# Kernel tuning notes

Measured on AMD Instinct MI355X. Metric: run time of the kernel, lower is better.

Reference implementation:

```python
import jax, jax.numpy as jnp
import numpy as np

B, S, D = 2, 2048, 1024
H = 16
HD = D // H  # 64


def setup_inputs() -> dict:
    key = jax.random.key(0)
    k = jax.random.split(key, 6)
    s = 0.02
    return {
        "x": jax.random.normal(k[0], (B, S, D), dtype=jnp.float32),
        "wq": jax.random.normal(k[1], (D, D), dtype=jnp.float32) * s,
        "wk": jax.random.normal(k[2], (D, D), dtype=jnp.float32) * s,
        "wv": jax.random.normal(k[3], (D, D), dtype=jnp.float32) * s,
        "wo": jax.random.normal(k[4], (D, D), dtype=jnp.float32) * s,
        "bo": jnp.zeros((D,), dtype=jnp.float32),
    }


def reference(x, wq, wk, wv, wo, bo):
    b, n, d = x.shape
    # nn.Linear: y = x @ W.T (qkv_bias=False)
    def proj(w):
        y = jnp.einsum('bnd,od->bno', x, w)
        return y.reshape(b, n, H, HD).transpose(0, 2, 1, 3)  # (b, H, n, hd)
    q, k, v = proj(wq), proj(wk), proj(wv)
    scores = jnp.einsum('bhqd,bhkd->bhqk', q, k) / jnp.sqrt(jnp.float32(HD))
    # NOTE: source code slices the causal mask but never applies it; softmax is unmasked.
    attn = jax.nn.softmax(scores, axis=-1)
    # dropout p=0.0 -> identity
    ctx = jnp.einsum('bhqk,bhkd->bhqd', attn, v)
    ctx = ctx.transpose(0, 2, 1, 3).reshape(b, n, d)
    return jnp.einsum('bnd,od->bno', ctx, wo) + bo
```

## Files before the change

### kernel.cpp

```cpp
#include <hip/hip_runtime.h>
#include <hip/hip_bf16.h>
#include <stdint.h>

typedef __attribute__((ext_vector_type(8))) short short8;
typedef __attribute__((ext_vector_type(4))) float float4v;
typedef __attribute__((ext_vector_type(4))) unsigned short ushort4v;
typedef __attribute__((ext_vector_type(4))) unsigned int uint4v;

#define Bq 2
#define Sq 2048
#define Dq 1024
#define Hq 16
#define HDq 64

#define QSCALE 0.18033688011112042f

__device__ __forceinline__ unsigned short f2bf(float f) {
  union { float f; uint32_t u; } v; v.f = f;
  uint32_t r = (v.u + 0x7FFFu + ((v.u >> 16) & 1u)) >> 16;
  return (unsigned short)r;
}

__device__ __forceinline__ uint32_t pk2bf(float a, float b) {
  union { __hip_bfloat162 h; uint32_t u; } cv;
  cv.h = __float22bfloat162_rn(make_float2(a, b));
  return cv.u;
}

__device__ __forceinline__ void gl_lds16(const unsigned short* g, unsigned short* l) {
  __builtin_amdgcn_global_load_lds(
      (const __attribute__((address_space(1))) void*)g,
      (__attribute__((address_space(3))) void*)l, 16, 0, 0);
}

__global__ __launch_bounds__(256) void cvt_all_kernel(
    const float* __restrict__ x,
    const float* __restrict__ w0, const float* __restrict__ w1,
    const float* __restrict__ w2, const float* __restrict__ w3,
    unsigned short* __restrict__ xb, unsigned short* __restrict__ wb) {
  const int bid = blockIdx.x;
  const float* src;
  unsigned short* dst;
  int idx;
  if (bid < 4096) {
    src = x; dst = xb;
    idx = bid * 256 + threadIdx.x;
  } else {
    int j = (bid - 4096) * 256 + threadIdx.x;
    int z = j >> 18;
    src = (z == 0) ? w0 : (z == 1) ? w1 : (z == 2) ? w2 : w3;
    dst = wb + (size_t)z * 1048576;
    idx = j & 262143;
  }
  float4v f = ((const float4v*)src)[idx];
  ushort4v o;
#pragma unroll
  for (int q = 0; q < 4; q++) o[q] = f2bf(f[q]);
  ((ushort4v*)dst)[idx] = o;
}

template <bool OUTPROJ, int MT>
__global__ __launch_bounds__(256) void gemm_bt_kernel(
    const unsigned short* __restrict__ A,
    const unsigned short* __restrict__ W0,
    const unsigned short* __restrict__ W1,
    const unsigned short* __restrict__ W2,
    unsigned short* __restrict__ q_dst,
    unsigned short* __restrict__ k_dst,
    unsigned short* __restrict__ v_dst,
    float* __restrict__ f_dst,
    const float* __restrict__ bias) {
  constexpr int K = 1024;
  constexpr int NMB = MT / 32;
  constexpr int APASS = MT / 32;
  const int z = blockIdx.z;
  const unsigned short* W = (z == 0) ? W0 : (z == 1) ? W1 : W2;
  unsigned short* qkv = (z == 0) ? q_dst : (z == 1) ? k_dst : v_dst;

  __shared__ unsigned short Asm[MT * 64];
  __shared__ unsigned short Bsm[128 * 64];

  const int t = threadIdx.x;
  const int wave = t >> 6, lane = t & 63;
  const int quad = lane >> 4, l16 = lane & 15;
  const int wy = wave >> 1, wx = wave & 1;
  const int row0 = blockIdx.x * MT;
  const int col0 = blockIdx.y * 128;

  float4v zero = {0.f, 0.f, 0.f, 0.f};
  float4v acc[NMB][4];
#pragma unroll
  for (int i = 0; i < NMB; i++)
#pragma unroll
    for (int j = 0; j < 4; j++) acc[i][j] = zero;

  const int srow = t >> 3;
  const int sgl = ((t & 7) ^ (srow & 7)) << 3;
  const unsigned short* gA[APASS];
  const unsigned short* gB[4];
#pragma unroll
  for (int i = 0; i < APASS; i++)
    gA[i] = A + (size_t)(row0 + i * 32 + srow) * K + sgl;
#pragma unroll
  for (int i = 0; i < 4; i++)
    gB[i] = W + (size_t)(col0 + i * 32 + srow) * K + sgl;

  const int swl = (l16 & 7);

  for (int k0 = 0; k0 < K; k0 += 64) {
#pragma unroll
    for (int i = 0; i < APASS; i++) gl_lds16(gA[i] + k0, &Asm[i * 2048 + t * 8]);
#pragma unroll
    for (int i = 0; i < 4; i++) gl_lds16(gB[i] + k0, &Bsm[i * 2048 + t * 8]);
    __syncthreads();
    short8 af[NMB][2], bf[4][2];
#pragma unroll
    for (int ks = 0; ks < 2; ks++) {
#pragma unroll
      for (int mb = 0; mb < NMB; mb++) {
        int row = wy * (MT / 2) + mb * 16 + l16;
        int pg = (ks * 4 + quad) ^ swl;
        af[mb][ks] = *(const short8*)(&Asm[row * 64 + pg * 8]);
      }
#pragma unroll
      for (int nb = 0; nb < 4; nb++) {
        int row = wx * 64 + nb * 16 + l16;
        int pg = (ks * 4 + quad) ^ swl;
        bf[nb][ks] = *(const short8*)(&Bsm[row * 64 + pg * 8]);
      }
    }
#pragma unroll
    for (int ks = 0; ks < 2; ks++)
#pragma unroll
      for (int mb = 0; mb < NMB; mb++)
#pragma unroll
        for (int nb = 0; nb < 4; nb++)
          acc[mb][nb] = __builtin_amdgcn_mfma_f32_16x16x32_bf16(af[mb][ks], bf[nb][ks], acc[mb][nb], 0, 0, 0);
    __syncthreads();
  }

  const float qsc = (!OUTPROJ && z == 0) ? QSCALE : 1.0f;
#pragma unroll
  for (int mb = 0; mb < NMB; mb++) {
#pragma unroll
    for (int nb = 0; nb < 4; nb++) {
#pragma unroll
      for (int r = 0; r < 4; r++) {
        int row = row0 + wy * (MT / 2) + mb * 16 + quad * 4 + r;
        int o = col0 + wx * 64 + nb * 16 + l16;
        float val = acc[mb][nb][r];
        if (OUTPROJ) {
          f_dst[(size_t)row * 1024 + o] = val + bias[o];
        } else {
          int b = row >> 11, s = row & 2047;
          int h = o >> 6, hd = o & 63;
          qkv[(size_t)((b * Hq + h) * Sq + s) * HDq + hd] = f2bf(val * qsc);
        }
      }
    }
  }
}

__global__ __launch_bounds__(256) void attn_kernel(
    const unsigned short* __restrict__ Q,
    const unsigned short* __restrict__ Kg,
    const unsigned short* __restrict__ Vg,
    unsigned short* __restrict__ ctx) {
  constexpr int VSTR = 136;
  constexpr int KBUF = 8192;
  constexpr int VBUF = 8704;
  __shared__ __align__(16) unsigned char smem[67584];
  unsigned short* Ksm = (unsigned short*)smem;
  unsigned short* Vsm = (unsigned short*)(smem + 32768);
  float* obuf = (float*)smem;
  float* dbuf = (float*)(smem + 34816);

  const int bh = blockIdx.y;
  const int q0 = blockIdx.x * 128;
  const int t = threadIdx.x;
  const int wave = t >> 6, lane = t & 63;
  const int quad = lane >> 4, l16 = lane & 15;
  const int wq = wave >> 1, wk = wave & 1;
  const int swl = l16 & 7;

  const unsigned short* Qb = Q + (size_t)bh * Sq * HDq;
  const unsigned short* Kb = Kg + (size_t)bh * Sq * HDq;
  const unsigned short* Vb = Vg + (size_t)bh * Sq * HDq;

  short8 qf[4][2];
#pragma unroll
  for (int qb = 0; qb < 4; qb++)
#pragma unroll
    for (int ks = 0; ks < 2; ks++)
      qf[qb][ks] = *(const short8*)(Qb + (size_t)(q0 + wq * 64 + qb * 16 + l16) * HDq + ks * 32 + quad * 8);

  short8 ones;
#pragma unroll
  for (int j = 0; j < 8; j++) ones[j] = (short)0x3F80;

  float4v zero = {0.f, 0.f, 0.f, 0.f};
  float4v of[4][4];
  float4v dsum[4];
#pragma unroll
  for (int qb = 0; qb < 4; qb++) {
    dsum[qb] = zero;
#pragma unroll
    for (int hb = 0; hb < 4; hb++) of[qb][hb] = zero;
  }

  const int srow = t >> 3;
  const unsigned short* gK = Kb + (size_t)srow * 64 + (((t & 7) ^ (srow & 7)) << 3);

  const int vr2 = (t & 63) * 2;
  const int vc16 = (t >> 6) << 4;
  const int sig = (vr2 & ~31) + (((vr2 >> 2) & 3) << 3) + (((vr2 >> 4) & 1) << 2) + (vr2 & 3);
  const unsigned short* gV = Vb + (size_t)vr2 * 64 + vc16;

  uint4v va0, va1, vb0, vb1;

#define VLOAD(off) do {                                            \
    const unsigned short* vp = gV + (size_t)(off) * 64;            \
    va0 = *(const uint4v*)(vp);      vb0 = *(const uint4v*)(vp + 8); \
    va1 = *(const uint4v*)(vp + 64); vb1 = *(const uint4v*)(vp + 72); \
  } while (0)

#define VPACK(bufsel) do {                                                   \
    unsigned short* vd = &Vsm[(bufsel) * VBUF + sig];                        \
    _Pragma("unroll")                                                        \
    for (int r = 0; r < 4; r++) {                                            \
      uint32_t w0 = __builtin_amdgcn_perm(va1[r], va0[r], 0x05040100u);      \
      uint32_t w1 = __builtin_amdgcn_perm(va1[r], va0[r], 0x07060302u);      \
      *(uint32_t*)(vd + (vc16 + 2 * r) * VSTR) = w0;                         \
      *(uint32_t*)(vd + (vc16 + 2 * r + 1) * VSTR) = w1;                     \
      uint32_t x0 = __builtin_amdgcn_perm(vb1[r], vb0[r], 0x05040100u);      \
      uint32_t x1 = __builtin_amdgcn_perm(vb1[r], vb0[r], 0x07060302u);      \
      *(uint32_t*)(vd + (vc16 + 8 + 2 * r) * VSTR) = x0;                     \
      *(uint32_t*)(vd + (vc16 + 8 + 2 * r + 1) * VSTR) = x1;                 \
    }                                                                        \
  } while (0)

#define KISSUE(off, bufsel) do {                                   \
    _Pragma("unroll")                                              \
    for (int i = 0; i < 4; i++)                                    \
      gl_lds16(gK + (size_t)(off) * 64 + i * 2048,                 \
               &Ksm[(bufsel) * KBUF + i * 2048 + t * 8]);          \
  } while (0)

  KISSUE(0, 0);
  VLOAD(0);
  VPACK(0);
  VLOAD(128);
  __syncthreads();
  KISSUE(128, 1);

  for (int kt = 0; kt < Sq; kt += 128) {
    const int cur = (kt >> 7) & 1;
#pragma unroll
    for (int p = 0; p < 2; p++) {
      const int kb0 = cur * KBUF + (wk * 64 + p * 32) * 64;
      short8 kf[2][2];
#pragma unroll
      for (int s = 0; s < 2; s++)
#pragma unroll
        for (int ks = 0; ks < 2; ks++)
          kf[s][ks] = *(const short8*)&Ksm[kb0 + (s * 16 + l16) * 64 + ((ks * 4 + quad) ^ swl) * 8];
      short8 pf[4];
#pragma unroll
      for (int qb = 0; qb < 4; qb++) {
        float4v s0 = zero, s1 = zero;
#pragma unroll
        for (int ks = 0; ks < 2; ks++) {
          s0 = __builtin_amdgcn_mfma_f32_16x16x32_bf16(kf[0][ks], qf[qb][ks], s0, 0, 0, 0);
          s1 = __builtin_amdgcn_mfma_f32_16x16x32_bf16(kf[1][ks], qf[qb][ks], s1, 0, 0, 0);
        }
        union { uint32_t u[4]; short8 v; } pw;
        pw.u[0] = pk2bf(__builtin_amdgcn_exp2f(s0[0]), __builtin_amdgcn_exp2f(s0[1]));
        pw.u[1] = pk2bf(__builtin_amdgcn_exp2f(s0[2]), __builtin_amdgcn_exp2f(s0[3]));
        pw.u[2] = pk2bf(__builtin_amdgcn_exp2f(s1[0]), __builtin_amdgcn_exp2f(s1[1]));
        pw.u[3] = pk2bf(__builtin_amdgcn_exp2f(s1[2]), __builtin_amdgcn_exp2f(s1[3]));
        pf[qb] = pw.v;
      }
#pragma unroll
      for (int qb = 0; qb < 4; qb++)
        dsum[qb] = __builtin_amdgcn_mfma_f32_16x16x32_bf16(pf[qb], ones, dsum[qb], 0, 0, 0);
      const int vbo = cur * VBUF + wk * 64 + p * 32 + quad * 8;
#pragma unroll
      for (int hb = 0; hb < 4; hb++) {
        short8 vf = *(const short8*)&Vsm[vbo + (hb * 16 + l16) * VSTR];
#pragma unroll
        for (int qb = 0; qb < 4; qb++)
          of[qb][hb] = __builtin_amdgcn_mfma_f32_16x16x32_bf16(pf[qb], vf, of[qb][hb], 0, 0, 0);
      }
    }
    if (kt + 128 < Sq) VPACK(cur ^ 1);
    if (kt + 256 < Sq) VLOAD(kt + 256);
    __syncthreads();
    if (kt + 256 < Sq) KISSUE(kt + 256, cur);
  }

  if (wk == 0) {
#pragma unroll
    for (int qb = 0; qb < 4; qb++) {
#pragma unroll
      for (int hb = 0; hb < 4; hb++)
        *(float4v*)&obuf[(wq * 64 + hb * 16 + l16) * 68 + qb * 16 + quad * 4] = of[qb][hb];
      if (l16 == 0)
#pragma unroll
        for (int r = 0; r < 4; r++)
          dbuf[wq * 64 + qb * 16 + quad * 4 + r] = dsum[qb][r];
    }
  }
  __syncthreads();
  if (wk == 1) {
#pragma unroll
    for (int qb = 0; qb < 4; qb++) {
#pragma unroll
      for (int hb = 0; hb < 4; hb++) {
        float4v* pp = (float4v*)&obuf[(wq * 64 + hb * 16 + l16) * 68 + qb * 16 + quad * 4];
        float4v o = *pp;
        o += of[qb][hb];
        *pp = o;
      }
      if (l16 == 0)
#pragma unroll
        for (int r = 0; r < 4; r++)
          dbuf[wq * 64 + qb * 16 + quad * 4 + r] += dsum[qb][r];
    }
  }
  __syncthreads();

  const int b = bh >> 4, h = bh & 15;
  const int qq = t & 127, hseg = t >> 7;
  const float dinv = 1.0f / dbuf[qq];
  const float* ob = &obuf[(qq >> 6) * 4352 + (hseg * 32) * 68 + (qq & 63)];
  unsigned short* cp = ctx + ((size_t)(b * Sq + q0 + qq)) * Dq + h * 64 + hseg * 32;
#pragma unroll
  for (int g = 0; g < 4; g++) {
    short8 o8;
#pragma unroll
    for (int j = 0; j < 8; j++) o8[j] = (short)f2bf(ob[(g * 8 + j) * 68] * dinv);
    *(short8*)(cp + g * 8) = o8;
  }
#undef VLOAD
#undef VPACK
#undef KISSUE
}

extern "C" void kernel_launch(void* const* d_in, const int* in_sizes, int n_in,
                              void* d_out, int out_size, void* d_ws, size_t ws_size,
                              hipStream_t stream) {
  (void)in_sizes; (void)n_in; (void)out_size; (void)ws_size;
  const float* x  = (const float*)d_in[0];
  const float* wq = (const float*)d_in[1];
  const float* wk = (const float*)d_in[2];
  const float* wv = (const float*)d_in[3];
  const float* wo = (const float*)d_in[4];
  const float* bo = (const float*)d_in[5];
  float* out = (float*)d_out;

  char* ws = (char*)d_ws;
  const size_t MB = 1u << 20;
  unsigned short* xb  = (unsigned short*)(ws + 0 * MB);
  unsigned short* wqb = (unsigned short*)(ws + 8 * MB);
  unsigned short* wkb = (unsigned short*)(ws + 10 * MB);
  unsigned short* wvb = (unsigned short*)(ws + 12 * MB);
  unsigned short* wob = (unsigned short*)(ws + 14 * MB);
  unsigned short* qb  = (unsigned short*)(ws + 16 * MB);
  unsigned short* kb  = (unsigned short*)(ws + 24 * MB);
  unsigned short* vb  = (unsigned short*)(ws + 32 * MB);
  unsigned short* cxb = (unsigned short*)(ws + 40 * MB);

  cvt_all_kernel<<<8192, 256, 0, stream>>>(x, wq, wk, wv, wo, xb, wqb);

  gemm_bt_kernel<false, 128><<<dim3(32, 8, 3), 256, 0, stream>>>(
      xb, wqb, wkb, wvb, qb, kb, vb, nullptr, nullptr);
  attn_kernel<<<dim3(16, 32), 256, 0, stream>>>(qb, kb, vb, cxb);
  gemm_bt_kernel<true, 64><<<dim3(64, 8, 1), 256, 0, stream>>>(
      cxb, wob, wob, wob, nullptr, nullptr, nullptr, out, bo);
}
```

Measured before the change: 192.8 us.

## Double attention block to 512 threads, halving queries per wave

The attention kernel now runs 8 waves per block instead of 4. Each wave owns 32 query rows instead of 64, which halves the per-wave Q fragments, output accumulators and row-sum registers. The K/V staging loads, the V transpose-pack and the final reduction and store are redistributed across the larger thread count, and the output buffer is relaid with a query-major stride. The aim is more resident waves to hide latency and lower register pressure per wave. The cost is that each wave now re-reads K and V fragments from LDS for half as many queries, doubling LDS read traffic per MFMA.

```diff
diff --git a/kernel.cpp b/kernel.cpp
--- a/kernel.cpp
+++ b/kernel.cpp
@@ -5,7 +5,6 @@
 typedef __attribute__((ext_vector_type(8))) short short8;
 typedef __attribute__((ext_vector_type(4))) float float4v;
 typedef __attribute__((ext_vector_type(4))) unsigned short ushort4v;
-typedef __attribute__((ext_vector_type(4))) unsigned int uint4v;
 
 #define Bq 2
 #define Sq 2048
@@ -161,7 +160,7 @@
   }
 }
 
-__global__ __launch_bounds__(256) void attn_kernel(
+__global__ __launch_bounds__(512, 4) void attn_kernel(
     const unsigned short* __restrict__ Q,
     const unsigned short* __restrict__ Kg,
     const unsigned short* __restrict__ Vg,
@@ -169,11 +168,12 @@
   constexpr int VSTR = 136;
   constexpr int KBUF = 8192;
   constexpr int VBUF = 8704;
+  constexpr int QSTR = 132;
   __shared__ __align__(16) unsigned char smem[67584];
   unsigned short* Ksm = (unsigned short*)smem;
   unsigned short* Vsm = (unsigned short*)(smem + 32768);
   float* obuf = (float*)smem;
-  float* dbuf = (float*)(smem + 34816);
+  float* dbuf = (float*)(smem + 33792);
 
   const int bh = blockIdx.y;
   const int q0 = blockIdx.x * 128;
@@ -187,22 +187,22 @@
   const unsigned short* Kb = Kg + (size_t)bh * Sq * HDq;
   const unsigned short* Vb = Vg + (size_t)bh * Sq * HDq;
 
-  short8 qf[4][2];
-#pragma unroll
-  for (int qb = 0; qb < 4; qb++)
+  short8 qf[2][2];
+#pragma unroll
+  for (int qb = 0; qb < 2; qb++)
 #pragma unroll
     for (int ks = 0; ks < 2; ks++)
-      qf[qb][ks] = *(const short8*)(Qb + (size_t)(q0 + wq * 64 + qb * 16 + l16) * HDq + ks * 32 + quad * 8);
+      qf[qb][ks] = *(const short8*)(Qb + (size_t)(q0 + wq * 32 + qb * 16 + l16) * HDq + ks * 32 + quad * 8);
 
   short8 ones;
 #pragma unroll
   for (int j = 0; j < 8; j++) ones[j] = (short)0x3F80;
 
   float4v zero = {0.f, 0.f, 0.f, 0.f};
-  float4v of[4][4];
-  float4v dsum[4];
-#pragma unroll
-  for (int qb = 0; qb < 4; qb++) {
+  float4v of[2][4];
+  float4v dsum[2];
+#pragma unroll
+  for (int qb = 0; qb < 2; qb++) {
     dsum[qb] = zero;
 #pragma unroll
     for (int hb = 0; hb < 4; hb++) of[qb][hb] = zero;
@@ -212,38 +212,32 @@
   const unsigned short* gK = Kb + (size_t)srow * 64 + (((t & 7) ^ (srow & 7)) << 3);
 
   const int vr2 = (t & 63) * 2;
-  const int vc16 = (t >> 6) << 4;
+  const int vc8 = (t >> 6) << 3;
   const int sig = (vr2 & ~31) + (((vr2 >> 2) & 3) << 3) + (((vr2 >> 4) & 1) << 2) + (vr2 & 3);
-  const unsigned short* gV = Vb + (size_t)vr2 * 64 + vc16;
-
-  uint4v va0, va1, vb0, vb1;
-
-#define VLOAD(off) do {                                            \
-    const unsigned short* vp = gV + (size_t)(off) * 64;            \
-    va0 = *(const uint4v*)(vp);      vb0 = *(const uint4v*)(vp + 8); \
-    va1 = *(const uint4v*)(vp + 64); vb1 = *(const uint4v*)(vp + 72); \
+  const unsigned short* gV = Vb + (size_t)vr2 * HDq + vc8;
+
+  short8 vpr0, vpr1;
+
+#define VLOAD(off) do {                                              \
+    const unsigned short* vp = gV + (size_t)(off) * HDq;             \
+    vpr0 = *(const short8*)(vp);                                     \
+    vpr1 = *(const short8*)(vp + HDq);                               \
   } while (0)
 
-#define VPACK(bufsel) do {                                                   \
-    unsigned short* vd = &Vsm[(bufsel) * VBUF + sig];                        \
-    _Pragma("unroll")                                                        \
-    for (int r = 0; r < 4; r++) {                                            \
-      uint32_t w0 = __builtin_amdgcn_perm(va1[r], va0[r], 0x05040100u);      \
-      uint32_t w1 = __builtin_amdgcn_perm(va1[r], va0[r], 0x07060302u);      \
-      *(uint32_t*)(vd + (vc16 + 2 * r) * VSTR) = w0;                         \
-      *(uint32_t*)(vd + (vc16 + 2 * r + 1) * VSTR) = w1;                     \
-      uint32_t x0 = __builtin_amdgcn_perm(vb1[r], vb0[r], 0x05040100u);      \
-      uint32_t x1 = __builtin_amdgcn_perm(vb1[r], vb0[r], 0x07060302u);      \
-      *(uint32_t*)(vd + (vc16 + 8 + 2 * r) * VSTR) = x0;                     \
-      *(uint32_t*)(vd + (vc16 + 8 + 2 * r + 1) * VSTR) = x1;                 \
-    }                                                                        \
+#define VPACK(bufsel) do {                                           \
+    unsigned short* vd = &Vsm[(bufsel) * VBUF + sig];                \
+    _Pragma("unroll")                                                \
+    for (int j = 0; j < 8; j++) {                                    \
+      uint32_t pk = (uint32_t)(unsigned short)vpr0[j] |              \
+                    ((uint32_t)(unsigned short)vpr1[j] << 16);       \
+      *(uint32_t*)(vd + (vc8 + j) * VSTR) = pk;                      \
+    }                                                                \
   } while (0)
 
-#define KISSUE(off, bufsel) do {                                   \
-    _Pragma("unroll")                                              \
-    for (int i = 0; i < 4; i++)                                    \
-      gl_lds16(gK + (size_t)(off) * 64 + i * 2048,                 \
-               &Ksm[(bufsel) * KBUF + i * 2048 + t * 8]);          \
+#define KISSUE(off, bufsel) do {                                     \
+    gl_lds16(gK + (size_t)(off) * 64, &Ksm[(bufsel) * KBUF + t * 8]);\
+    gl_lds16(gK + (size_t)(off) * 64 + 4096,                         \
+             &Ksm[(bufsel) * KBUF + 4096 + t * 8]);                  \
   } while (0)
 
   KISSUE(0, 0);
@@ -257,38 +251,38 @@
     const int cur = (kt >> 7) & 1;
 #pragma unroll
     for (int p = 0; p < 2; p++) {
-      const int kb0 = cur * KBUF + (wk * 64 + p * 32) * 64;
+      const int kb0 = cur * KBUF + wk * 4096 + p * 2048;
       short8 kf[2][2];
 #pragma unroll
       for (int s = 0; s < 2; s++)
 #pragma unroll
         for (int ks = 0; ks < 2; ks++)
           kf[s][ks] = *(const short8*)&Ksm[kb0 + (s * 16 + l16) * 64 + ((ks * 4 + quad) ^ swl) * 8];
-      short8 pf[4];
-#pragma unroll
-      for (int qb = 0; qb < 4; qb++) {
-        float4v s0 = zero, s1 = zero;
+      short8 pf[2];
+#pragma unroll
+      for (int qb = 0; qb < 2; qb++) {
+        float4v sa = zero, sb = zero;
 #pragma unroll
         for (int ks = 0; ks < 2; ks++) {
-          s0 = __builtin_amdgcn_mfma_f32_16x16x32_bf16(kf[0][ks], qf[qb][ks], s0, 0, 0, 0);
-          s1 = __builtin_amdgcn_mfma_f32_16x16x32_bf16(kf[1][ks], qf[qb][ks], s1, 0, 0, 0);
+          sa = __builtin_amdgcn_mfma_f32_16x16x32_bf16(kf[0][ks], qf[qb][ks], sa, 0, 0, 0);
+          sb = __builtin_amdgcn_mfma_f32_16x16x32_bf16(kf[1][ks], qf[qb][ks], sb, 0, 0, 0);
         }
         union { uint32_t u[4]; short8 v; } pw;
-        pw.u[0] = pk2bf(__builtin_amdgcn_exp2f(s0[0]), __builtin_amdgcn_exp2f(s0[1]));
-        pw.u[1] = pk2bf(__builtin_amdgcn_exp2f(s0[2]), __builtin_amdgcn_exp2f(s0[3]));
-        pw.u[2] = pk2bf(__builtin_amdgcn_exp2f(s1[0]), __builtin_amdgcn_exp2f(s1[1]));
-        pw.u[3] = pk2bf(__builtin_amdgcn_exp2f(s1[2]), __builtin_amdgcn_exp2f(s1[3]));
+        pw.u[0] = pk2bf(__builtin_amdgcn_exp2f(sa[0]), __builtin_amdgcn_exp2f(sa[1]));
+        pw.u[1] = pk2bf(__builtin_amdgcn_exp2f(sa[2]), __builtin_amdgcn_exp2f(sa[3]));
+        pw.u[2] = pk2bf(__builtin_amdgcn_exp2f(sb[0]), __builtin_amdgcn_exp2f(sb[1]));
+        pw.u[3] = pk2bf(__builtin_amdgcn_exp2f(sb[2]), __builtin_amdgcn_exp2f(sb[3]));
         pf[qb] = pw.v;
       }
 #pragma unroll
-      for (int qb = 0; qb < 4; qb++)
+      for (int qb = 0; qb < 2; qb++)
         dsum[qb] = __builtin_amdgcn_mfma_f32_16x16x32_bf16(pf[qb], ones, dsum[qb], 0, 0, 0);
       const int vbo = cur * VBUF + wk * 64 + p * 32 + quad * 8;
 #pragma unroll
       for (int hb = 0; hb < 4; hb++) {
         short8 vf = *(const short8*)&Vsm[vbo + (hb * 16 + l16) * VSTR];
 #pragma unroll
-        for (int qb = 0; qb < 4; qb++)
+        for (int qb = 0; qb < 2; qb++)
           of[qb][hb] = __builtin_amdgcn_mfma_f32_16x16x32_bf16(pf[qb], vf, of[qb][hb], 0, 0, 0);
       }
     }
@@ -300,23 +294,23 @@
 
   if (wk == 0) {
 #pragma unroll
-    for (int qb = 0; qb < 4; qb++) {
+    for (int qb = 0; qb < 2; qb++) {
 #pragma unroll
       for (int hb = 0; hb < 4; hb++)
-        *(float4v*)&obuf[(wq * 64 + hb * 16 + l16) * 68 + qb * 16 + quad * 4] = of[qb][hb];
+        *(float4v*)&obuf[(hb * 16 + l16) * QSTR + wq * 32 + qb * 16 + quad * 4] = of[qb][hb];
       if (l16 == 0)
 #pragma unroll
         for (int r = 0; r < 4; r++)
-          dbuf[wq * 64 + qb * 16 + quad * 4 + r] = dsum[qb][r];
+          dbuf[wq * 32 + qb * 16 + quad * 4 + r] = dsum[qb][r];
     }
   }
   __syncthreads();
   if (wk == 1) {
 #pragma unroll
-    for (int qb = 0; qb < 4; qb++) {
+    for (int qb = 0; qb < 2; qb++) {
 #pragma unroll
       for (int hb = 0; hb < 4; hb++) {
-        float4v* pp = (float4v*)&obuf[(wq * 64 + hb * 16 + l16) * 68 + qb * 16 + quad * 4];
+        float4v* pp = (float4v*)&obuf[(hb * 16 + l16) * QSTR + wq * 32 + qb * 16 + quad * 4];
         float4v o = *pp;
         o += of[qb][hb];
         *pp = o;
@@ -324,7 +318,7 @@
       if (l16 == 0)
 #pragma unroll
         for (int r = 0; r < 4; r++)
-          dbuf[wq * 64 + qb * 16 + quad * 4 + r] += dsum[qb][r];
+          dbuf[wq * 32 + qb * 16 + quad * 4 + r] += dsum[qb][r];
     }
   }
   __syncthreads();
@@ -332,15 +326,14 @@
   const int b = bh >> 4, h = bh & 15;
   const int qq = t & 127, hseg = t >> 7;
   const float dinv = 1.0f / dbuf[qq];
-  const float* ob = &obuf[(qq >> 6) * 4352 + (hseg * 32) * 68 + (qq & 63)];
-  unsigned short* cp = ctx + ((size_t)(b * Sq + q0 + qq)) * Dq + h * 64 + hseg * 32;
-#pragma unroll
-  for (int g = 0; g < 4; g++) {
-    short8 o8;
-#pragma unroll
-    for (int j = 0; j < 8; j++) o8[j] = (short)f2bf(ob[(g * 8 + j) * 68] * dinv);
-    *(short8*)(cp + g * 8) = o8;
-  }
+  unsigned short* cp = ctx + ((size_t)(b * Sq + q0 + qq)) * Dq + h * 64 + hseg * 16;
+  short8 o8a, o8b;
+#pragma unroll
+  for (int j = 0; j < 8; j++) o8a[j] = (short)f2bf(obuf[(hseg * 16 + j) * QSTR + qq] * dinv);
+#pragma unroll
+  for (int j = 0; j < 8; j++) o8b[j] = (short)f2bf(obuf[(hseg * 16 + 8 + j) * QSTR + qq] * dinv);
+  *(short8*)cp = o8a;
+  *(short8*)(cp + 8) = o8b;
 #undef VLOAD
 #undef VPACK
 #undef KISSUE
@@ -374,7 +367,7 @@
 
   gemm_bt_kernel<false, 128><<<dim3(32, 8, 3), 256, 0, stream>>>(
       xb, wqb, wkb, wvb, qb, kb, vb, nullptr, nullptr);
-  attn_kernel<<<dim3(16, 32), 256, 0, stream>>>(qb, kb, vb, cxb);
+  attn_kernel<<<dim3(16, 32), 512, 0, stream>>>(qb, kb, vb, cxb);
   gemm_bt_kernel<true, 64><<<dim3(64, 8, 1), 256, 0, stream>>>(
       cxb, wob, wob, wob, nullptr, nullptr, nullptr, out, bo);
 }
```

Result: faster. 184.2 us (-4.5%).
